# Performance work log

Hardware: AMD Instinct MI355X
Metric: run time of the kernel (lower is better)

## Reference

```python
import math
import jax, jax.numpy as jnp
import numpy as np

D_MODEL = 1024
D_STATE = 16
D_CONV = 4
EXPAND = 2
N_MOD = 2
D_INNER = EXPAND * D_MODEL
DT_RANK = math.ceil(D_MODEL / 16)
B_SZ = 2
SEQLEN = 2048


def setup_inputs() -> dict:
    key = jax.random.key(0)
    ks = jax.random.split(key, 10)
    hidden_states = jax.random.normal(ks[0], (B_SZ, SEQLEN, D_MODEL), jnp.float32)
    modality_ids = jax.random.randint(ks[1], (B_SZ, SEQLEN), 0, N_MOD).astype(jnp.int32)
    W_in = jax.random.normal(ks[2], (N_MOD, 2 * D_INNER, D_MODEL), jnp.float32) * (D_MODEL ** -0.5)
    conv_w = jax.random.normal(ks[3], (D_INNER, D_CONV), jnp.float32) * (D_CONV ** -0.5)
    conv_b = jnp.zeros((D_INNER,), jnp.float32)
    W_x = jax.random.normal(ks[4], (N_MOD, DT_RANK + 2 * D_STATE, D_INNER), jnp.float32) * (D_INNER ** -0.5)
    dt_init_std = DT_RANK ** -0.5
    W_dt = jax.random.uniform(ks[5], (N_MOD, D_INNER, DT_RANK), jnp.float32, -dt_init_std, dt_init_std)
    # dt bias init: inverse-softplus of dt ~ LogUniform(dt_min, dt_max), per Mamba
    dt = jnp.exp(jax.random.uniform(ks[6], (N_MOD, D_INNER), jnp.float32)
                 * (math.log(0.1) - math.log(0.001)) + math.log(0.001))
    dt = jnp.maximum(dt, 1e-4)
    b_dt = dt + jnp.log(-jnp.expm1(-dt))
    A_log = jnp.log(jnp.broadcast_to(jnp.arange(1, D_STATE + 1, dtype=jnp.float32), (D_INNER, D_STATE)))
    D = jnp.ones((D_INNER,), jnp.float32)
    W_out = jax.random.normal(ks[7], (N_MOD, D_MODEL, D_INNER), jnp.float32) * (D_INNER ** -0.5)
    return dict(hidden_states=hidden_states, modality_ids=modality_ids, W_in=W_in,
                conv_w=conv_w, conv_b=conv_b, W_x=W_x, W_dt=W_dt, b_dt=b_dt,
                A_log=A_log, D=D, W_out=W_out)


def _expert_apply(x, W, ids):
    # x: [T, d_in], W: [E, d_out, d_in], ids: [T] -> per-token expert output [T, d_out]
    all_out = jnp.einsum('td,eod->teo', x, W)
    return jnp.take_along_axis(all_out, ids[:, None, None], axis=1)[:, 0, :]


def _forward(hidden_states, modality_ids, W_in, conv_w, conv_b, W_x, W_dt, b_dt, A_log, D, W_out):
    Bsz, L, d_model = hidden_states.shape
    d_inner, d_state = A_log.shape
    dt_rank = W_dt.shape[2]
    d_conv = conv_w.shape[1]
    ids = modality_ids.reshape(-1)  # [T]

    # per-modality in_proj dispatch/combine
    xz = _expert_apply(hidden_states.reshape(-1, d_model), W_in, ids)  # [T, 2*d_inner]
    xz = xz.reshape(Bsz, L, 2 * d_inner).transpose(0, 2, 1)            # [B, 2*d_inner, L]
    x, z = jnp.split(xz, 2, axis=1)                                    # [B, d_inner, L] each

    # causal depthwise conv1d (pad left d_conv-1, truncate to L) + SiLU
    xp = jnp.pad(x, ((0, 0), (0, 0), (d_conv - 1, 0)))
    xc = conv_b[None, :, None]
    for k in range(d_conv):
        xc = xc + conv_w[None, :, k:k + 1] * xp[:, :, k:k + L]
    x = jax.nn.silu(xc)

    # per-modality x_proj -> (dt, B, C)
    xt = x.transpose(0, 2, 1).reshape(-1, d_inner)                     # [T, d_inner]
    x_dbl = _expert_apply(xt, W_x, ids)
    dt, Bm, Cm = jnp.split(x_dbl, [dt_rank, dt_rank + d_state], axis=-1)

    # per-modality dt_proj (with bias), then softplus (delta_softplus=True)
    dt = _expert_apply(dt, W_dt, ids) + b_dt[ids]                      # [T, d_inner]
    dt = jax.nn.softplus(dt)

    A = -jnp.exp(A_log)                                                # [d_inner, d_state]

    # selective scan over sequence (time-major)
    dts = dt.reshape(Bsz, L, d_inner).transpose(1, 0, 2)               # [L, B, d_inner]
    Bms = Bm.reshape(Bsz, L, d_state).transpose(1, 0, 2)               # [L, B, d_state]
    Cms = Cm.reshape(Bsz, L, d_state).transpose(1, 0, 2)               # [L, B, d_state]
    xs = x.transpose(2, 0, 1)                                          # [L, B, d_inner]

    def step(state, inp):
        x_t, dt_t, B_t, C_t = inp
        dA = jnp.exp(dt_t[..., None] * A)                              # [B, d_inner, d_state]
        state = state * dA + (dt_t * x_t)[..., None] * B_t[:, None, :]
        y_t = jnp.einsum('bdn,bn->bd', state, C_t)
        return state, y_t

    init = jnp.zeros((Bsz, d_inner, d_state), jnp.float32)
    _, ys = jax.lax.scan(step, init, (xs, dts, Bms, Cms))              # ys: [L, B, d_inner]

    y = ys.transpose(1, 0, 2)                                          # [B, L, d_inner]
    y = y + x.transpose(0, 2, 1) * D[None, None, :]                    # skip D*u
    y = y * jax.nn.silu(z.transpose(0, 2, 1))                          # z gate

    # per-modality out_proj
    out = _expert_apply(y.reshape(-1, d_inner), W_out, ids)
    return out.reshape(Bsz, L, d_model)


def reference(hidden_states, modality_ids, W_in, conv_w, conv_b, W_x, W_dt, b_dt, A_log, D, W_out):
    return _forward(hidden_states, modality_ids, W_in, conv_w, conv_b, W_x, W_dt, b_dt, A_log, D, W_out)
```

## Files before the change

### kernel.cpp

```cpp
#include <hip/hip_runtime.h>
#include <hip/hip_bf16.h>
#include <math.h>

#define B_SZ 2
#define SEQLEN 2048
#define D_MODEL 1024
#define D_INNER 2048
#define D_STATE 16
#define D_CONV 4
#define DT_RANK 64
#define NTOK (B_SZ * SEQLEN)
#define XDBL 96
#define NC 32
#define LC 64
#define PADTOT (34 * 128)

typedef float f32x4 __attribute__((ext_vector_type(4)));
typedef unsigned int u32x4 __attribute__((ext_vector_type(4)));
typedef __hip_bfloat16 bf16;

__device__ __forceinline__ float siluf(float v) { return v / (1.f + __expf(-v)); }
__device__ __forceinline__ float softplusf(float v) { return (v > 20.f) ? v : log1pf(__expf(v)); }

__device__ __forceinline__ void mfma_bf16(f32x4& acc, u32x4 a, u32x4 b) {
  asm("v_mfma_f32_16x16x32_bf16 %0, %1, %2, %0" : "+v"(acc) : "v"(a), "v"(b));
}

__device__ __forceinline__ void gload16(const bf16* g, bf16* l) {
  __builtin_amdgcn_global_load_lds(
      (const __attribute__((address_space(1))) unsigned int*)g,
      (__attribute__((address_space(3))) unsigned int*)l, 16, 0, 0);
}

__global__ __launch_bounds__(1024) void k_perm(const int* __restrict__ ids, int* __restrict__ perm) {
  __shared__ int sc[1024];
  const int tid = threadIdx.x;
  int loc[4];
  int cnt = 0;
#pragma unroll
  for (int q = 0; q < 4; q++) {
    loc[q] = ids[tid * 4 + q];
    cnt += (loc[q] == 0);
  }
  sc[tid] = cnt;
  __syncthreads();
  for (int off = 1; off < 1024; off <<= 1) {
    int v = sc[tid];
    int u = (tid >= off) ? sc[tid - off] : 0;
    __syncthreads();
    sc[tid] = v + u;
    __syncthreads();
  }
  const int N0 = sc[1023];
  const int m0 = (N0 + 127) & ~127;
  const int N1 = NTOK - N0;
  for (int idx = tid; idx < PADTOT; idx += 1024)
    if ((idx >= N0 && idx < m0) || idx >= m0 + N1) perm[idx] = -1;
  int zb = sc[tid] - cnt;
#pragma unroll
  for (int q = 0; q < 4; q++) {
    int t = tid * 4 + q;
    if (loc[q] == 0) { perm[zb] = t; zb++; }
    else             { perm[m0 + (t - zb)] = t; }
  }
}

#define CVT_H   (NTOK * D_MODEL)
#define CVT_WIN (2 * 2 * D_INNER * D_MODEL)
#define CVT_WX  (2 * XDBL * D_INNER)
#define CVT_WDT (2 * D_INNER * DT_RANK)
#define CVT_WO  (2 * D_MODEL * D_INNER)
#define CVT_TOT (CVT_H + CVT_WIN + CVT_WX + CVT_WDT + CVT_WO)
__global__ __launch_bounds__(256) void k_cvtall(const float* __restrict__ h,
                                                const float* __restrict__ Win,
                                                const float* __restrict__ Wx,
                                                const float* __restrict__ Wdt,
                                                const float* __restrict__ Wout,
                                                bf16* __restrict__ hB, bf16* __restrict__ WinB,
                                                bf16* __restrict__ WxB, bf16* __restrict__ WdtB,
                                                bf16* __restrict__ WoB) {
  size_t i = ((size_t)blockIdx.x * 256 + threadIdx.x) * 8;
  const float* src; bf16* dst; size_t off;
  if (i < CVT_H)                          { src = h;    dst = hB;   off = i; }
  else if (i < CVT_H + CVT_WIN)           { src = Win;  dst = WinB; off = i - CVT_H; }
  else if (i < CVT_H + CVT_WIN + CVT_WX)  { src = Wx;   dst = WxB;  off = i - CVT_H - CVT_WIN; }
  else if (i < CVT_TOT - CVT_WO)          { src = Wdt;  dst = WdtB; off = i - CVT_H - CVT_WIN - CVT_WX; }
  else                                    { src = Wout; dst = WoB;  off = i - (CVT_TOT - CVT_WO); }
  float4 f0 = *(const float4*)&src[off];
  float4 f1 = *(const float4*)&src[off + 4];
  __align__(16) bf16 tmp[8];
  tmp[0] = __float2bfloat16(f0.x); tmp[1] = __float2bfloat16(f0.y);
  tmp[2] = __float2bfloat16(f0.z); tmp[3] = __float2bfloat16(f0.w);
  tmp[4] = __float2bfloat16(f1.x); tmp[5] = __float2bfloat16(f1.y);
  tmp[6] = __float2bfloat16(f1.z); tmp[7] = __float2bfloat16(f1.w);
  *(u32x4*)&dst[off] = *(const u32x4*)tmp;
}

template <int KDIM, int NW, int LDO, int EPI, int KSPLIT, int SWZ>
__global__ __launch_bounds__(256) void k_gemmG(const bf16* __restrict__ actB,
                                               const int* __restrict__ perm,
                                               const int* __restrict__ ids,
                                               const bf16* __restrict__ WB,
                                               const float* __restrict__ bias,
                                               float* __restrict__ out0,
                                               bf16* __restrict__ outb) {
  static_assert(KDIM % (64 * KSPLIT) == 0, "K split");
  constexpr int KLEN = KDIM / KSPLIT;
  __shared__ bf16 As[128 * 64];
  __shared__ bf16 Ws[128 * 64];
  __shared__ int permL[128];
  const int tid = threadIdx.x;

  int bx, by;
  if (SWZ) {
    const int gx = gridDim.x;
    const int nwg = gx * gridDim.y;
    const int fid = blockIdx.y * gx + blockIdx.x;
    const int q8 = nwg >> 3;
    const int swz = (fid & 7) * q8 + (fid >> 3);
    bx = swz % gx;
    by = swz / gx;
  } else {
    bx = blockIdx.x;
    by = blockIdx.y;
  }

  const int ot = (KSPLIT > 1) ? 0 : bx * 128;
  const int kz = (KSPLIT > 1) ? bx : 0;
  const int kbase = kz * KLEN;
  const int tt = by * 128;

  if (tid < 128) permL[tid] = perm[tt + tid];

  const int lane = tid & 63, w = tid >> 6;
  const int wr = w >> 1, wc = w & 1;
  const int lr = lane & 15, lg = lane >> 4;

  const int t00 = perm[tt];
  const int eu = (t00 >= 0) ? ids[t00] : 0;
  const size_t wexp = (size_t)eu * NW * KDIM;

  const int srow = w * 32 + (lane >> 3);
  const int scol = (lane & 7) * 8;
  size_t abase[4], bbase[4];
  int ldsoff[4];
#pragma unroll
  for (int v = 0; v < 4; v++) {
    const int row = srow + v * 8;
    int ta = perm[tt + row];
    if (ta < 0) ta = 0;
    abase[v] = (size_t)ta * KDIM + scol;
    int orow = ot + row;
    if (NW % 128 != 0) orow = (orow < NW) ? orow : (NW - 1);
    bbase[v] = wexp + (size_t)orow * KDIM + scol;
    ldsoff[v] = (w * 32 + v * 8) * 64;
  }

  f32x4 acc[4][4];
#pragma unroll
  for (int i = 0; i < 4; i++)
#pragma unroll
    for (int j = 0; j < 4; j++) acc[i][j] = (f32x4){0.f, 0.f, 0.f, 0.f};

  for (int k0 = kbase; k0 < kbase + KLEN; k0 += 64) {
#pragma unroll
    for (int v = 0; v < 4; v++) {
      gload16(&actB[abase[v] + k0], &As[ldsoff[v]]);
      gload16(&WB[bbase[v] + k0], &Ws[ldsoff[v]]);
    }
    __syncthreads();
#pragma unroll
    for (int ks = 0; ks < 64; ks += 32) {
      u32x4 a[4], b[4];
#pragma unroll
      for (int f = 0; f < 4; f++)
        a[f] = *(const u32x4*)&As[(wr * 64 + f * 16 + lr) * 64 + ks + lg * 8];
#pragma unroll
      for (int f = 0; f < 4; f++)
        b[f] = *(const u32x4*)&Ws[(wc * 64 + f * 16 + lr) * 64 + ks + lg * 8];
#pragma unroll
      for (int i = 0; i < 4; i++)
#pragma unroll
        for (int j = 0; j < 4; j++) mfma_bf16(acc[i][j], a[i], b[j]);
    }
    __syncthreads();
  }

#pragma unroll
  for (int i = 0; i < 4; i++) {
#pragma unroll
    for (int r = 0; r < 4; r++) {
      const int m = wr * 64 + i * 16 + lg * 4 + r;
      const int t = permL[m];
      if (t < 0) continue;
#pragma unroll
      for (int j = 0; j < 4; j++) {
        const int col = ot + wc * 64 + j * 16 + lr;
        float v = acc[i][j][r];
        if (EPI == 0) {
          out0[(size_t)t * LDO + col] = v;
        } else if (EPI == 1) {
          if (col < D_INNER) out0[(size_t)t * D_INNER + col] = v;
          else outb[(size_t)t * D_INNER + (col - D_INNER)] = __float2bfloat16(v);
        } else if (EPI == 2) {
          v = softplusf(v + bias[eu * NW + col]);
          out0[(size_t)t * LDO + col] = v;
        } else if (EPI == 3) {
          if (col < XDBL) out0[((size_t)kz * NTOK + t) * XDBL + col] = v;
        }
      }
    }
  }
}

__global__ __launch_bounds__(256) void k_xred(const float* __restrict__ part,
                                              float* __restrict__ xdbl,
                                              bf16* __restrict__ x64B) {
  const int i = blockIdx.x * 256 + threadIdx.x;
  float s = 0.f;
#pragma unroll
  for (int k = 0; k < 8; k++) s += part[(size_t)k * NTOK * XDBL + i];
  xdbl[i] = s;
  const int t = i / XDBL, col = i - t * XDBL;
  if (col < DT_RANK) x64B[(size_t)t * DT_RANK + col] = __float2bfloat16(s);
}

__global__ __launch_bounds__(256) void k_conv(const float* __restrict__ x_raw,
                                              const float* __restrict__ cw,
                                              const float* __restrict__ cb,
                                              bf16* __restrict__ xB) {
  int idx = blockIdx.x * 256 + threadIdx.x;
  int c = idx & (D_INNER - 1);
  int t = idx >> 11;
  int l = t & (SEQLEN - 1);
  int b = t >> 11;
  float acc = cb[c];
#pragma unroll
  for (int k = 0; k < D_CONV; k++) {
    int ll = l + k - (D_CONV - 1);
    if (ll >= 0)
      acc = fmaf(cw[c * D_CONV + k], x_raw[((size_t)(b * SEQLEN + ll)) * D_INNER + c], acc);
  }
  xB[(size_t)idx] = __float2bfloat16(siluf(acc));
}

__global__ __launch_bounds__(256) void k_scan_part(const bf16* __restrict__ xB,
                                                   const float* __restrict__ dtb,
                                                   const float* __restrict__ xdbl,
                                                   const float* __restrict__ A_log,
                                                   float* __restrict__ F,
                                                   float* __restrict__ Sdt) {
  __shared__ float Bs[LC][D_STATE];
  const int tid = threadIdx.x;
  const int j = blockIdx.y;
  const int ch = blockIdx.x * 256 + tid;
  const int b = ch >> 11, c = ch & (D_INNER - 1);
  const int t0 = (b << 11) + j * LC;
  {
    int l = tid >> 2, q = (tid & 3) * 4;
    *(float4*)&Bs[l][q] = *(const float4*)&xdbl[(size_t)(t0 + l) * XDBL + DT_RANK + q];
  }
  float Ar[D_STATE];
#pragma unroll
  for (int n4 = 0; n4 < 4; n4++) {
    float4 a = *(const float4*)&A_log[(size_t)c * D_STATE + n4 * 4];
    Ar[n4 * 4 + 0] = -__expf(a.x); Ar[n4 * 4 + 1] = -__expf(a.y);
    Ar[n4 * 4 + 2] = -__expf(a.z); Ar[n4 * 4 + 3] = -__expf(a.w);
  }
  __syncthreads();
  float st[D_STATE];
#pragma unroll
  for (int n = 0; n < D_STATE; n++) st[n] = 0.f;
  float sdt = 0.f;
  float dtc = dtb[(size_t)t0 * D_INNER + c];
  float xc = __bfloat162float(xB[(size_t)t0 * D_INNER + c]);
  for (int l = 0; l < LC; l++) {
    float dtn = 0.f, xn = 0.f;
    if (l < LC - 1) {
      dtn = dtb[(size_t)(t0 + l + 1) * D_INNER + c];
      xn = __bfloat162float(xB[(size_t)(t0 + l + 1) * D_INNER + c]);
    }
    const float dtx = dtc * xc;
    sdt += dtc;
#pragma unroll
    for (int n = 0; n < D_STATE; n++) {
      float dA = __expf(dtc * Ar[n]);
      st[n] = fmaf(st[n], dA, dtx * Bs[l][n]);
    }
    dtc = dtn; xc = xn;
  }
  const size_t fb = ((size_t)j * NTOK + ch) * D_STATE;
#pragma unroll
  for (int n4 = 0; n4 < 4; n4++)
    *(float4*)&F[fb + n4 * 4] = make_float4(st[n4 * 4], st[n4 * 4 + 1], st[n4 * 4 + 2], st[n4 * 4 + 3]);
  Sdt[(size_t)j * NTOK + ch] = sdt;
}

__global__ __launch_bounds__(256) void k_combine(const float* __restrict__ F,
                                                 const float* __restrict__ Sdt,
                                                 const float* __restrict__ A_log,
                                                 float* __restrict__ s0) {
  const int gid = blockIdx.x * 256 + threadIdx.x;
  const int ch = gid >> 4, n = gid & 15, c = ch & (D_INNER - 1);
  const float Ar = -__expf(A_log[(size_t)c * D_STATE + n]);
  float s = 0.f;
  for (int j = 0; j < NC; j++) {
    s0[((size_t)j * NTOK + ch) * D_STATE + n] = s;
    s = fmaf(s, __expf(Ar * Sdt[(size_t)j * NTOK + ch]), F[((size_t)j * NTOK + ch) * D_STATE + n]);
  }
}

__global__ __launch_bounds__(256) void k_scan_fin(const bf16* __restrict__ xB,
                                                  const float* __restrict__ dtb,
                                                  const float* __restrict__ xdbl,
                                                  const bf16* __restrict__ zB,
                                                  const float* __restrict__ A_log,
                                                  const float* __restrict__ Dp,
                                                  const float* __restrict__ s0,
                                                  bf16* __restrict__ ybuf) {
  __shared__ float Bs[LC][D_STATE];
  __shared__ float Cs[LC][D_STATE];
  const int tid = threadIdx.x;
  const int j = blockIdx.y;
  const int ch = blockIdx.x * 256 + tid;
  const int b = ch >> 11, c = ch & (D_INNER - 1);
  const int t0 = (b << 11) + j * LC;
  {
    int l = tid >> 2, q = (tid & 3) * 4;
    *(float4*)&Bs[l][q] = *(const float4*)&xdbl[(size_t)(t0 + l) * XDBL + DT_RANK + q];
    *(float4*)&Cs[l][q] = *(const float4*)&xdbl[(size_t)(t0 + l) * XDBL + DT_RANK + D_STATE + q];
  }
  float Ar[D_STATE];
#pragma unroll
  for (int n4 = 0; n4 < 4; n4++) {
    float4 a = *(const float4*)&A_log[(size_t)c * D_STATE + n4 * 4];
    Ar[n4 * 4 + 0] = -__expf(a.x); Ar[n4 * 4 + 1] = -__expf(a.y);
    Ar[n4 * 4 + 2] = -__expf(a.z); Ar[n4 * 4 + 3] = -__expf(a.w);
  }
  __syncthreads();
  float st[D_STATE];
  const size_t sb = ((size_t)j * NTOK + ch) * D_STATE;
#pragma unroll
  for (int n4 = 0; n4 < 4; n4++) {
    float4 s = *(const float4*)&s0[sb + n4 * 4];
    st[n4 * 4 + 0] = s.x; st[n4 * 4 + 1] = s.y; st[n4 * 4 + 2] = s.z; st[n4 * 4 + 3] = s.w;
  }
  const float Dc = Dp[c];
  float dtc = dtb[(size_t)t0 * D_INNER + c];
  float xc = __bfloat162float(xB[(size_t)t0 * D_INNER + c]);
  for (int l = 0; l < LC; l++) {
    float dtn = 0.f, xn = 0.f;
    if (l < LC - 1) {
      dtn = dtb[(size_t)(t0 + l + 1) * D_INNER + c];
      xn = __bfloat162float(xB[(size_t)(t0 + l + 1) * D_INNER + c]);
    }
    const float zv = __bfloat162float(zB[(size_t)(t0 + l) * D_INNER + c]);
    const float dtx = dtc * xc;
    float y = 0.f;
#pragma unroll
    for (int n = 0; n < D_STATE; n++) {
      float dA = __expf(dtc * Ar[n]);
      st[n] = fmaf(st[n], dA, dtx * Bs[l][n]);
      y = fmaf(st[n], Cs[l][n], y);
    }
    float yv = fmaf(xc, Dc, y);
    ybuf[(size_t)(t0 + l) * D_INNER + c] = __float2bfloat16(yv * siluf(zv));
    dtc = dtn; xc = xn;
  }
}

extern "C" void kernel_launch(void* const* d_in, const int* in_sizes, int n_in,
                              void* d_out, int out_size, void* d_ws, size_t ws_size,
                              hipStream_t stream) {
  const float* h = (const float*)d_in[0];
  const int* ids = (const int*)d_in[1];
  const float* Win = (const float*)d_in[2];
  const float* cw = (const float*)d_in[3];
  const float* cb = (const float*)d_in[4];
  const float* Wx = (const float*)d_in[5];
  const float* Wdt = (const float*)d_in[6];
  const float* bdt = (const float*)d_in[7];
  const float* Alog = (const float*)d_in[8];
  const float* Dp = (const float*)d_in[9];
  const float* Wout = (const float*)d_in[10];
  float* out = (float*)d_out;

  const size_t NTD = (size_t)NTOK * D_INNER;
  float* ws = (float*)d_ws;
  float* slot0 = ws + 0 * NTD;
  float* slot1 = ws + 1 * NTD;
  float* dtb_p = ws + 2 * NTD;
  float* xraw_p = ws + 3 * NTD;
  size_t cur = 4 * NTD;
  float* xdbl_p = ws + cur; cur += (size_t)NTOK * XDBL;
  float* sdt_p = ws + cur; cur += (size_t)NC * NTOK;
  int* perm = (int*)(ws + cur); cur += PADTOT;
  bf16* xB = (bf16*)(ws + cur); cur += NTD / 2;
  bf16* WoB = (bf16*)(ws + cur); cur += CVT_WO / 2;
  bf16* WxB = (bf16*)(ws + cur); cur += CVT_WX / 2;
  bf16* WdtB = (bf16*)(ws + cur); cur += CVT_WDT / 2;
  bf16* x64B = (bf16*)(ws + cur); cur += (size_t)NTOK * DT_RANK / 2;

  bf16* hB = (bf16*)slot0;
  bf16* zB = (bf16*)slot1;
  bf16* WinB = (bf16*)dtb_p;
  float* part = dtb_p;
  float* F = xraw_p;
  bf16* yB = (bf16*)xraw_p;
  float* s0 = (float*)d_out;

  k_perm<<<1, 1024, 0, stream>>>(ids, perm);
  k_cvtall<<<CVT_TOT / 8 / 256, 256, 0, stream>>>(h, Win, Wx, Wdt, Wout, hB, WinB, WxB, WdtB, WoB);
  k_gemmG<D_MODEL, 2 * D_INNER, 0, 1, 1, 1>
      <<<dim3(32, 34), 256, 0, stream>>>(hB, perm, ids, WinB, nullptr, xraw_p, zB);
  k_conv<<<NTD / 256, 256, 0, stream>>>(xraw_p, cw, cb, xB);
  k_gemmG<D_INNER, XDBL, XDBL, 3, 8, 0>
      <<<dim3(8, 34), 256, 0, stream>>>(xB, perm, ids, WxB, nullptr, part, nullptr);
  k_xred<<<NTOK * XDBL / 256, 256, 0, stream>>>(part, xdbl_p, x64B);
  k_gemmG<DT_RANK, D_INNER, D_INNER, 2, 1, 1>
      <<<dim3(16, 34), 256, 0, stream>>>(x64B, perm, ids, WdtB, bdt, dtb_p, nullptr);
  k_scan_part<<<dim3(16, NC), 256, 0, stream>>>(xB, dtb_p, xdbl_p, Alog, F, sdt_p);
  k_combine<<<256, 256, 0, stream>>>(F, sdt_p, Alog, s0);
  k_scan_fin<<<dim3(16, NC), 256, 0, stream>>>(xB, dtb_p, xdbl_p, zB, Alog, Dp, s0, yB);
  k_gemmG<D_INNER, D_MODEL, D_MODEL, 0, 1, 1>
      <<<dim3(8, 34), 256, 0, stream>>>(yB, perm, ids, WoB, nullptr, out, nullptr);
}
```

Before: 342.2 us.

## Double-buffer LDS tiles in grouped GEMM to overlap global loads with MFMA

Switches the grouped GEMM main loop to two LDS buffers. The next K tile is issued with direct-to-LDS loads while MFMAs run on the current tile, and a partial vmcnt wait plus a raw s_barrier replace the full __syncthreads. The per-block perm cache in LDS is dropped and the epilogue reads perm from global memory instead. This doubles the LDS footprint, which can lower occupancy, and it depends on the vmcnt count of 8 matching the number of loads issued per stage.

```diff
diff --git a/kernel.cpp b/kernel.cpp
--- a/kernel.cpp
+++ b/kernel.cpp
@@ -106,9 +106,9 @@
                                                bf16* __restrict__ outb) {
   static_assert(KDIM % (64 * KSPLIT) == 0, "K split");
   constexpr int KLEN = KDIM / KSPLIT;
-  __shared__ bf16 As[128 * 64];
-  __shared__ bf16 Ws[128 * 64];
-  __shared__ int permL[128];
+  constexpr int NT = KLEN / 64;
+  __shared__ bf16 As[2][128 * 64];
+  __shared__ bf16 Ws[2][128 * 64];
   const int tid = threadIdx.x;
 
   int bx, by;
@@ -130,8 +130,6 @@
   const int kbase = kz * KLEN;
   const int tt = by * 128;
 
-  if (tid < 128) permL[tid] = perm[tt + tid];
-
   const int lane = tid & 63, w = tid >> 6;
   const int wr = w >> 1, wc = w & 1;
   const int lr = lane & 15, lg = lane >> 4;
@@ -162,28 +160,42 @@
 #pragma unroll
     for (int j = 0; j < 4; j++) acc[i][j] = (f32x4){0.f, 0.f, 0.f, 0.f};
 
-  for (int k0 = kbase; k0 < kbase + KLEN; k0 += 64) {
+  auto STAGE = [&](int buf, int k0) {
 #pragma unroll
     for (int v = 0; v < 4; v++) {
-      gload16(&actB[abase[v] + k0], &As[ldsoff[v]]);
-      gload16(&WB[bbase[v] + k0], &Ws[ldsoff[v]]);
-    }
-    __syncthreads();
+      gload16(&actB[abase[v] + k0], &As[buf][ldsoff[v]]);
+      gload16(&WB[bbase[v] + k0], &Ws[buf][ldsoff[v]]);
+    }
+  };
+
+  STAGE(0, kbase);
+  int cur = 0;
+  for (int t = 0; t < NT; t++) {
+    if (t + 1 < NT) {
+      STAGE(cur ^ 1, kbase + (t + 1) * 64);
+      asm volatile("s_waitcnt vmcnt(8)" ::: "memory");
+    } else {
+      asm volatile("s_waitcnt vmcnt(0)" ::: "memory");
+    }
+    __builtin_amdgcn_s_barrier();
+    const bf16* Ab = As[cur];
+    const bf16* Wb = Ws[cur];
 #pragma unroll
     for (int ks = 0; ks < 64; ks += 32) {
       u32x4 a[4], b[4];
 #pragma unroll
       for (int f = 0; f < 4; f++)
-        a[f] = *(const u32x4*)&As[(wr * 64 + f * 16 + lr) * 64 + ks + lg * 8];
+        a[f] = *(const u32x4*)&Ab[(wr * 64 + f * 16 + lr) * 64 + ks + lg * 8];
 #pragma unroll
       for (int f = 0; f < 4; f++)
-        b[f] = *(const u32x4*)&Ws[(wc * 64 + f * 16 + lr) * 64 + ks + lg * 8];
+        b[f] = *(const u32x4*)&Wb[(wc * 64 + f * 16 + lr) * 64 + ks + lg * 8];
 #pragma unroll
       for (int i = 0; i < 4; i++)
 #pragma unroll
         for (int j = 0; j < 4; j++) mfma_bf16(acc[i][j], a[i], b[j]);
     }
-    __syncthreads();
+    __builtin_amdgcn_s_barrier();
+    cur ^= 1;
   }
 
 #pragma unroll
@@ -191,7 +203,7 @@
 #pragma unroll
     for (int r = 0; r < 4; r++) {
       const int m = wr * 64 + i * 16 + lg * 4 + r;
-      const int t = permL[m];
+      const int t = perm[tt + m];
       if (t < 0) continue;
 #pragma unroll
       for (int j = 0; j < 4; j++) {
```

After: 395.4 us. +15.5%, slower.

## Add 256-row triple-buffered in_proj GEMM and store x_raw and dt in bf16

Applied to the files above, without the earlier changes.

Replaces the generic in_proj GEMM with a dedicated 512-thread kernel that uses 256x128 tiles, three LDS stages with explicit vmcnt waits and split load issue, and setprio around the MFMA blocks. Expert padding is raised to 256 rows so each tile stays within one modality. The in_proj x output and the softplus dt output are now written as bf16 rather than fp32, which halves the traffic for the conv and both scan passes but costs precision in dt and x_raw. Workspace slots are reassigned to fit the new bf16 buffers.

```diff
diff --git a/kernel.cpp b/kernel.cpp
--- a/kernel.cpp
+++ b/kernel.cpp
@@ -13,7 +13,7 @@
 #define XDBL 96
 #define NC 32
 #define LC 64
-#define PADTOT (34 * 128)
+#define PADTOT (17 * 256)
 
 typedef float f32x4 __attribute__((ext_vector_type(4)));
 typedef unsigned int u32x4 __attribute__((ext_vector_type(4)));
@@ -23,7 +23,7 @@
 __device__ __forceinline__ float softplusf(float v) { return (v > 20.f) ? v : log1pf(__expf(v)); }
 
 __device__ __forceinline__ void mfma_bf16(f32x4& acc, u32x4 a, u32x4 b) {
-  asm("v_mfma_f32_16x16x32_bf16 %0, %1, %2, %0" : "+v"(acc) : "v"(a), "v"(b));
+  asm volatile("v_mfma_f32_16x16x32_bf16 %0, %1, %2, %0" : "+v"(acc) : "v"(a), "v"(b));
 }
 
 __device__ __forceinline__ void gload16(const bf16* g, bf16* l) {
@@ -52,7 +52,7 @@
     __syncthreads();
   }
   const int N0 = sc[1023];
-  const int m0 = (N0 + 127) & ~127;
+  const int m0 = (N0 + 255) & ~255;
   const int N1 = NTOK - N0;
   for (int idx = tid; idx < PADTOT; idx += 1024)
     if ((idx >= N0 && idx < m0) || idx >= m0 + N1) perm[idx] = -1;
@@ -96,6 +96,157 @@
   *(u32x4*)&dst[off] = *(const u32x4*)tmp;
 }
 
+__global__ __launch_bounds__(512) void k_gemmP(const bf16* __restrict__ actB,
+                                               const int* __restrict__ perm,
+                                               const int* __restrict__ ids,
+                                               const bf16* __restrict__ WB,
+                                               bf16* __restrict__ outx,
+                                               bf16* __restrict__ outz) {
+  constexpr int KDIM = D_MODEL;
+  constexpr int NW = 2 * D_INNER;
+  constexpr int NT = KDIM / 64;
+  __shared__ bf16 As[3][256 * 64];
+  __shared__ bf16 Ws[3][128 * 64];
+  const int tid = threadIdx.x;
+
+  const int gx = gridDim.x;
+  const int nwg = gx * gridDim.y;
+  const int fid = blockIdx.y * gx + blockIdx.x;
+  const int q8 = nwg >> 3;
+  const int swz = (fid & 7) * q8 + (fid >> 3);
+  const int bx = swz % gx, by = swz / gx;
+  const int ot = bx * 128;
+  const int tt = by * 256;
+
+  const int lane = tid & 63, w = tid >> 6;
+  const int wr = w >> 1, wc = w & 1;
+  const int lr = lane & 15, lg = lane >> 4;
+
+  const int t00 = perm[tt];
+  const int eu = (t00 >= 0) ? ids[t00] : 0;
+  const size_t wexp = (size_t)eu * NW * KDIM;
+
+  const int kswz = ((lane & 7) ^ ((lane >> 3) & 7)) * 8;
+  size_t aBase[4]; int aLds[4];
+  size_t bBase[2]; int bLds[2];
+#pragma unroll
+  for (int v = 0; v < 4; v++) {
+    const int row = w * 32 + v * 8 + (lane >> 3);
+    int ta = perm[tt + row]; if (ta < 0) ta = 0;
+    aBase[v] = (size_t)ta * KDIM + kswz;
+    aLds[v] = (w * 32 + v * 8) * 64;
+  }
+#pragma unroll
+  for (int v = 0; v < 2; v++) {
+    const int row = w * 16 + v * 8 + (lane >> 3);
+    bBase[v] = wexp + (size_t)(ot + row) * KDIM + kswz;
+    bLds[v] = (w * 16 + v * 8) * 64;
+  }
+
+  f32x4 acc[4][4];
+#pragma unroll
+  for (int i = 0; i < 4; i++)
+#pragma unroll
+    for (int j = 0; j < 4; j++) acc[i][j] = (f32x4){0.f, 0.f, 0.f, 0.f};
+
+#pragma unroll
+  for (int kt = 0; kt < 2; kt++) {
+    const int k0 = kt * 64;
+    gload16(&actB[aBase[0] + k0], &As[kt][aLds[0]]);
+    gload16(&actB[aBase[1] + k0], &As[kt][aLds[1]]);
+    gload16(&actB[aBase[2] + k0], &As[kt][aLds[2]]);
+    gload16(&actB[aBase[3] + k0], &As[kt][aLds[3]]);
+    gload16(&WB[bBase[0] + k0], &Ws[kt][bLds[0]]);
+    gload16(&WB[bBase[1] + k0], &Ws[kt][bLds[1]]);
+  }
+
+  int bR = 0, bS = 2;
+  for (int kt = 0; kt < NT; ++kt) {
+    const int kp = (kt + 2) * 64;
+    const bool st = (kt + 2 < NT);
+    if (st) {
+      gload16(&actB[aBase[0] + kp], &As[bS][aLds[0]]);
+      gload16(&actB[aBase[1] + kp], &As[bS][aLds[1]]);
+      gload16(&WB[bBase[0] + kp], &Ws[bS][bLds[0]]);
+    }
+    if (kt < NT - 2)       asm volatile("s_waitcnt vmcnt(9)" ::: "memory");
+    else if (kt == NT - 2) asm volatile("s_waitcnt vmcnt(6)" ::: "memory");
+    else                   asm volatile("s_waitcnt vmcnt(0)" ::: "memory");
+    asm volatile("s_barrier" ::: "memory");
+
+    const bf16* Ab = As[bR];
+    const bf16* Wb = Ws[bR];
+    u32x4 a[4][2], b0[2][2];
+#pragma unroll
+    for (int f = 0; f < 4; f++)
+#pragma unroll
+      for (int s = 0; s < 2; s++) {
+        const int row = wr * 64 + f * 16 + lr;
+        a[f][s] = *(const u32x4*)&Ab[row * 64 + ((s * 4 + lg) ^ (row & 7)) * 8];
+      }
+#pragma unroll
+    for (int j = 0; j < 2; j++)
+#pragma unroll
+      for (int s = 0; s < 2; s++) {
+        const int row = wc * 64 + j * 16 + lr;
+        b0[j][s] = *(const u32x4*)&Wb[row * 64 + ((s * 4 + lg) ^ (row & 7)) * 8];
+      }
+    __builtin_amdgcn_s_setprio(1);
+#pragma unroll
+    for (int f = 0; f < 4; f++)
+#pragma unroll
+      for (int j = 0; j < 2; j++) {
+        mfma_bf16(acc[f][j], a[f][0], b0[j][0]);
+        mfma_bf16(acc[f][j], a[f][1], b0[j][1]);
+      }
+    __builtin_amdgcn_s_setprio(0);
+
+    if (st) {
+      gload16(&actB[aBase[2] + kp], &As[bS][aLds[2]]);
+      gload16(&actB[aBase[3] + kp], &As[bS][aLds[3]]);
+      gload16(&WB[bBase[1] + kp], &Ws[bS][bLds[1]]);
+    }
+    u32x4 b1[2][2];
+#pragma unroll
+    for (int j = 0; j < 2; j++)
+#pragma unroll
+      for (int s = 0; s < 2; s++) {
+        const int row = wc * 64 + (2 + j) * 16 + lr;
+        b1[j][s] = *(const u32x4*)&Wb[row * 64 + ((s * 4 + lg) ^ (row & 7)) * 8];
+      }
+    __builtin_amdgcn_s_setprio(1);
+#pragma unroll
+    for (int f = 0; f < 4; f++)
+#pragma unroll
+      for (int j = 0; j < 2; j++) {
+        mfma_bf16(acc[f][2 + j], a[f][0], b1[j][0]);
+        mfma_bf16(acc[f][2 + j], a[f][1], b1[j][1]);
+      }
+    __builtin_amdgcn_s_setprio(0);
+    asm volatile("s_waitcnt lgkmcnt(0)" ::: "memory");
+    asm volatile("s_barrier" ::: "memory");
+    bR = (bR == 2) ? 0 : bR + 1;
+    bS = (bS == 2) ? 0 : bS + 1;
+  }
+
+#pragma unroll
+  for (int i = 0; i < 4; i++) {
+#pragma unroll
+    for (int r = 0; r < 4; r++) {
+      const int m = wr * 64 + i * 16 + lg * 4 + r;
+      const int t = perm[tt + m];
+      if (t < 0) continue;
+#pragma unroll
+      for (int j = 0; j < 4; j++) {
+        const int col = ot + wc * 64 + j * 16 + lr;
+        const bf16 v = __float2bfloat16(acc[i][j][r]);
+        if (col < D_INNER) outx[(size_t)t * D_INNER + col] = v;
+        else outz[(size_t)t * D_INNER + (col - D_INNER)] = v;
+      }
+    }
+  }
+}
+
 template <int KDIM, int NW, int LDO, int EPI, int KSPLIT, int SWZ>
 __global__ __launch_bounds__(256) void k_gemmG(const bf16* __restrict__ actB,
                                                const int* __restrict__ perm,
@@ -199,12 +350,9 @@
         float v = acc[i][j][r];
         if (EPI == 0) {
           out0[(size_t)t * LDO + col] = v;
-        } else if (EPI == 1) {
-          if (col < D_INNER) out0[(size_t)t * D_INNER + col] = v;
-          else outb[(size_t)t * D_INNER + (col - D_INNER)] = __float2bfloat16(v);
         } else if (EPI == 2) {
           v = softplusf(v + bias[eu * NW + col]);
-          out0[(size_t)t * LDO + col] = v;
+          outb[(size_t)t * LDO + col] = __float2bfloat16(v);
         } else if (EPI == 3) {
           if (col < XDBL) out0[((size_t)kz * NTOK + t) * XDBL + col] = v;
         }
@@ -225,7 +373,7 @@
   if (col < DT_RANK) x64B[(size_t)t * DT_RANK + col] = __float2bfloat16(s);
 }
 
-__global__ __launch_bounds__(256) void k_conv(const float* __restrict__ x_raw,
+__global__ __launch_bounds__(256) void k_conv(const bf16* __restrict__ xrawB,
                                               const float* __restrict__ cw,
                                               const float* __restrict__ cb,
                                               bf16* __restrict__ xB) {
@@ -239,13 +387,14 @@
   for (int k = 0; k < D_CONV; k++) {
     int ll = l + k - (D_CONV - 1);
     if (ll >= 0)
-      acc = fmaf(cw[c * D_CONV + k], x_raw[((size_t)(b * SEQLEN + ll)) * D_INNER + c], acc);
+      acc = fmaf(cw[c * D_CONV + k],
+                 __bfloat162float(xrawB[((size_t)(b * SEQLEN + ll)) * D_INNER + c]), acc);
   }
   xB[(size_t)idx] = __float2bfloat16(siluf(acc));
 }
 
 __global__ __launch_bounds__(256) void k_scan_part(const bf16* __restrict__ xB,
-                                                   const float* __restrict__ dtb,
+                                                   const bf16* __restrict__ dtB,
                                                    const float* __restrict__ xdbl,
                                                    const float* __restrict__ A_log,
                                                    float* __restrict__ F,
@@ -272,12 +421,12 @@
 #pragma unroll
   for (int n = 0; n < D_STATE; n++) st[n] = 0.f;
   float sdt = 0.f;
-  float dtc = dtb[(size_t)t0 * D_INNER + c];
+  float dtc = __bfloat162float(dtB[(size_t)t0 * D_INNER + c]);
   float xc = __bfloat162float(xB[(size_t)t0 * D_INNER + c]);
   for (int l = 0; l < LC; l++) {
     float dtn = 0.f, xn = 0.f;
     if (l < LC - 1) {
-      dtn = dtb[(size_t)(t0 + l + 1) * D_INNER + c];
+      dtn = __bfloat162float(dtB[(size_t)(t0 + l + 1) * D_INNER + c]);
       xn = __bfloat162float(xB[(size_t)(t0 + l + 1) * D_INNER + c]);
     }
     const float dtx = dtc * xc;
@@ -311,7 +460,7 @@
 }
 
 __global__ __launch_bounds__(256) void k_scan_fin(const bf16* __restrict__ xB,
-                                                  const float* __restrict__ dtb,
+                                                  const bf16* __restrict__ dtB,
                                                   const float* __restrict__ xdbl,
                                                   const bf16* __restrict__ zB,
                                                   const float* __restrict__ A_log,
@@ -346,12 +495,12 @@
     st[n4 * 4 + 0] = s.x; st[n4 * 4 + 1] = s.y; st[n4 * 4 + 2] = s.z; st[n4 * 4 + 3] = s.w;
   }
   const float Dc = Dp[c];
-  float dtc = dtb[(size_t)t0 * D_INNER + c];
+  float dtc = __bfloat162float(dtB[(size_t)t0 * D_INNER + c]);
   float xc = __bfloat162float(xB[(size_t)t0 * D_INNER + c]);
   for (int l = 0; l < LC; l++) {
     float dtn = 0.f, xn = 0.f;
     if (l < LC - 1) {
-      dtn = dtb[(size_t)(t0 + l + 1) * D_INNER + c];
+      dtn = __bfloat162float(dtB[(size_t)(t0 + l + 1) * D_INNER + c]);
       xn = __bfloat162float(xB[(size_t)(t0 + l + 1) * D_INNER + c]);
     }
     const float zv = __bfloat162float(zB[(size_t)(t0 + l) * D_INNER + c]);
@@ -389,8 +538,8 @@
   float* ws = (float*)d_ws;
   float* slot0 = ws + 0 * NTD;
   float* slot1 = ws + 1 * NTD;
-  float* dtb_p = ws + 2 * NTD;
-  float* xraw_p = ws + 3 * NTD;
+  float* slot2 = ws + 2 * NTD;
+  float* slot3 = ws + 3 * NTD;
   size_t cur = 4 * NTD;
   float* xdbl_p = ws + cur; cur += (size_t)NTOK * XDBL;
   float* sdt_p = ws + cur; cur += (size_t)NC * NTOK;
@@ -402,26 +551,27 @@
   bf16* x64B = (bf16*)(ws + cur); cur += (size_t)NTOK * DT_RANK / 2;
 
   bf16* hB = (bf16*)slot0;
+  bf16* dtbB = (bf16*)slot0;
   bf16* zB = (bf16*)slot1;
-  bf16* WinB = (bf16*)dtb_p;
-  float* part = dtb_p;
-  float* F = xraw_p;
-  bf16* yB = (bf16*)xraw_p;
+  bf16* WinB = (bf16*)slot2;
+  float* part = slot2;
+  bf16* xrawB = (bf16*)slot3;
+  float* F = slot3;
+  bf16* yB = (bf16*)slot3;
   float* s0 = (float*)d_out;
 
   k_perm<<<1, 1024, 0, stream>>>(ids, perm);
   k_cvtall<<<CVT_TOT / 8 / 256, 256, 0, stream>>>(h, Win, Wx, Wdt, Wout, hB, WinB, WxB, WdtB, WoB);
-  k_gemmG<D_MODEL, 2 * D_INNER, 0, 1, 1, 1>
-      <<<dim3(32, 34), 256, 0, stream>>>(hB, perm, ids, WinB, nullptr, xraw_p, zB);
-  k_conv<<<NTD / 256, 256, 0, stream>>>(xraw_p, cw, cb, xB);
+  k_gemmP<<<dim3(32, 17), 512, 0, stream>>>(hB, perm, ids, WinB, xrawB, zB);
+  k_conv<<<NTD / 256, 256, 0, stream>>>(xrawB, cw, cb, xB);
   k_gemmG<D_INNER, XDBL, XDBL, 3, 8, 0>
       <<<dim3(8, 34), 256, 0, stream>>>(xB, perm, ids, WxB, nullptr, part, nullptr);
   k_xred<<<NTOK * XDBL / 256, 256, 0, stream>>>(part, xdbl_p, x64B);
   k_gemmG<DT_RANK, D_INNER, D_INNER, 2, 1, 1>
-      <<<dim3(16, 34), 256, 0, stream>>>(x64B, perm, ids, WdtB, bdt, dtb_p, nullptr);
-  k_scan_part<<<dim3(16, NC), 256, 0, stream>>>(xB, dtb_p, xdbl_p, Alog, F, sdt_p);
+      <<<dim3(16, 34), 256, 0, stream>>>(x64B, perm, ids, WdtB, bdt, nullptr, dtbB);
+  k_scan_part<<<dim3(16, NC), 256, 0, stream>>>(xB, dtbB, xdbl_p, Alog, F, sdt_p);
   k_combine<<<256, 256, 0, stream>>>(F, sdt_p, Alog, s0);
-  k_scan_fin<<<dim3(16, NC), 256, 0, stream>>>(xB, dtb_p, xdbl_p, zB, Alog, Dp, s0, yB);
+  k_scan_fin<<<dim3(16, NC), 256, 0, stream>>>(xB, dtbB, xdbl_p, zB, Alog, Dp, s0, yB);
   k_gemmG<D_INNER, D_MODEL, D_MODEL, 0, 1, 1>
       <<<dim3(8, 34), 256, 0, stream>>>(yB, perm, ids, WoB, nullptr, out, nullptr);
 }
```

New measurement: 357.6 us. +4.5%, slower.
